# Kernel optimization log

Measured on AMD Instinct MI355X. Metric: run time of the kernel, lower is better.

The kernel has to match this reference:

```python
import jax, jax.numpy as jnp
import numpy as np

MAX_REL = 128  # max_relative_position


def setup_inputs() -> dict:
    key = jax.random.key(0)
    k1, k2, k3, k4 = jax.random.split(key, 4)
    B, H, S, D = 2, 8, 2048, 64
    q = jax.random.normal(k1, (B, H, S, D), dtype=jnp.float32)
    k = jax.random.normal(k2, (B, H, S, D), dtype=jnp.float32)
    v = jax.random.normal(k3, (B, H, S, D), dtype=jnp.float32)
    rel_table = jax.random.normal(k4, (2 * MAX_REL + 1, D), dtype=jnp.float32)
    return {"q": q, "k": k, "v": v, "rel_table": rel_table}


def reference(q, k, v, rel_table):
    B, H, S, D = q.shape
    scale = jnp.sqrt(jnp.asarray(D, q.dtype))
    # content scores: [B,H,S,S]
    qk_scores = jnp.einsum('bhqd,bhkd->bhqk', q, k)
    # relative position index matrix [S,S] clamped to [-MAX_REL, MAX_REL]
    pos = jnp.arange(S)
    rel_idx = jnp.clip(pos[None, :] - pos[:, None], -MAX_REL, MAX_REL) + MAX_REL
    rel_emb = rel_table[rel_idx]  # [S,S,D]
    # relative scores: per-query dot with rel embedding row -> [B,H,S,S]
    rel_scores = jnp.einsum('bhqd,qkd->bhqk', q, rel_emb)
    scores = (qk_scores + rel_scores) / scale
    attn = jax.nn.softmax(scores, axis=-1)
    # output: [B,H,S,D]
    return jnp.einsum('bhqk,bhkd->bhqd', attn, v)
```

## Files before the change

kernel.cpp:

```cpp
#include <hip/hip_runtime.h>

typedef _Float16 half8 __attribute__((ext_vector_type(8)));
typedef _Float16 half4 __attribute__((ext_vector_type(4)));
typedef float f32x4 __attribute__((ext_vector_type(4)));

#define S_LEN 2048
#define HDIM 64
#define QBLK 64
#define KVBLK 64
#define NT (S_LEN / KVBLK)
#define QRS 258
#define NBH 16
#define L2E 1.44269504f
#define TSTR 72

__device__ __forceinline__ void load_lds16(const void* g, void* l) {
    __builtin_amdgcn_global_load_lds(
        (const __attribute__((address_space(1))) unsigned int*)g,
        (__attribute__((address_space(3))) unsigned int*)l, 16, 0, 0);
}

__global__ __launch_bounds__(256)
void convert_kv_kernel(const float* __restrict__ Kg, const float* __restrict__ Vg,
                       _Float16* __restrict__ Kh, _Float16* __restrict__ Vp)
{
    __shared__ _Float16 tile[KVBLK * TSTR];
    const int bid = blockIdx.x;
    const int tid = threadIdx.x;
    if (bid < 1024) {
        const int id = bid * 256 + tid;
        const int r  = id >> 3;
        const int d0 = (id & 7) * 8;
        const float* src = Kg + (size_t)r * HDIM + d0;
        f32x4 f0 = *(const f32x4*)(src);
        f32x4 f1 = *(const f32x4*)(src + 4);
        half8 h;
#pragma unroll
        for (int j = 0; j < 4; ++j) { h[j] = (_Float16)f0[j]; h[j+4] = (_Float16)f1[j]; }
        const int bh = r >> 11, kvg = r & 2047;
        const int t = kvg >> 6, kv = kvg & 63;
        const size_t blk = (size_t)(bh * NT + t) * 8192;
        const int off = (kv * 128 + d0 * 2) ^ ((kv & 7) << 4);
        *(half8*)((char*)Kh + blk + off) = h;
    } else {
        const int bt = bid - 1024;
        const int bh = bt >> 5, t = bt & 31;
        {
            const int kv = tid >> 2;
            const int d0 = (tid & 3) * 16;
            const float* src = Vg + ((size_t)bh * S_LEN + t * KVBLK + kv) * HDIM + d0;
            f32x4 f0 = *(const f32x4*)(src);
            f32x4 f1 = *(const f32x4*)(src + 4);
            f32x4 f2 = *(const f32x4*)(src + 8);
            f32x4 f3 = *(const f32x4*)(src + 12);
            half8 h0, h1;
#pragma unroll
            for (int j = 0; j < 4; ++j) {
                h0[j] = (_Float16)f0[j]; h0[j+4] = (_Float16)f1[j];
                h1[j] = (_Float16)f2[j]; h1[j+4] = (_Float16)f3[j];
            }
            *(half8*)&tile[kv * TSTR + d0]     = h0;
            *(half8*)&tile[kv * TSTR + d0 + 8] = h1;
        }
        __syncthreads();
        {
            const int dp = tid >> 2;
            const int u0 = (tid & 3) * 2;
            char* base = (char*)Vp + (size_t)bt * 8192;
            const int dsw = (dp & 7) << 4;
#pragma unroll
            for (int ui = 0; ui < 2; ++ui) {
                const int u  = u0 + ui;
                const int kc = u >> 2, gg = u & 3;
                half8 ch;
#pragma unroll
                for (int r = 0; r < 4; ++r) {
                    ch[r]     = tile[(32*kc + 4*gg + r)      * TSTR + dp];
                    ch[4 + r] = tile[(32*kc + 16 + 4*gg + r) * TSTR + dp];
                }
                *(half8*)(base + ((dp * 128 + u * 16) ^ dsw)) = ch;
            }
        }
    }
}

__global__ __launch_bounds__(512, 4)
void relattn_v7(const float* __restrict__ Qg, const float* __restrict__ RELg,
                const _Float16* __restrict__ Kh, const _Float16* __restrict__ Vp,
                float* __restrict__ Og)
{
    __shared__ __attribute__((aligned(16))) _Float16 Kbuf[2][4096];
    __shared__ __attribute__((aligned(16))) _Float16 Vbuf[2][4096];
    __shared__ __attribute__((aligned(16))) _Float16 Qrel[QBLK * QRS];
    __shared__ float MLds[2][64];
    __shared__ float LLds[2][64];

    const int tid  = threadIdx.x;
    const int wave = tid >> 6;
    const int lane = tid & 63;
    const int c  = lane & 15;
    const int g  = lane >> 4;
    const int qs = wave & 3;
    const int ks = wave >> 2;

    const int wk = ((blockIdx.x & 7) << 6) + (blockIdx.x >> 3);
    const int bh = wk >> 5;
    const int q0 = (wk & 31) * QBLK;
    const size_t hoff = (size_t)bh * S_LEN * HDIM;

    const int qb0 = q0 + 16 * qs;
    half8 bq[2];
#pragma unroll
    for (int kc = 0; kc < 2; ++kc) {
        const float* src = Qg + hoff + (size_t)(qb0 + c) * HDIM + kc * 32 + g * 8;
        f32x4 f0 = *(const f32x4*)(src);
        f32x4 f1 = *(const f32x4*)(src + 4);
        half8 h;
#pragma unroll
        for (int j = 0; j < 4; ++j) {
            h[j]     = (_Float16)(f0[j] * 0.125f);
            h[j + 4] = (_Float16)(f1[j] * 0.125f);
        }
        bq[kc] = h;
    }

    if (ks == 0) {
#pragma unroll 1
        for (int t = 0; t < 17; ++t) {
            f32x4 acc = {0.f, 0.f, 0.f, 0.f};
            int r = t * 16 + c;
            if (r > 256) r = 256;
#pragma unroll
            for (int kc = 0; kc < 2; ++kc) {
                const float* src = RELg + (size_t)r * HDIM + kc * 32 + g * 8;
                f32x4 f0 = *(const f32x4*)(src);
                f32x4 f1 = *(const f32x4*)(src + 4);
                half8 b;
#pragma unroll
                for (int j = 0; j < 4; ++j) { b[j] = (_Float16)f0[j]; b[j+4] = (_Float16)f1[j]; }
                acc = __builtin_amdgcn_mfma_f32_16x16x32_f16(bq[kc], b, acc, 0, 0, 0);
            }
            const int col = t * 16 + c;
            if (col <= 256) {
#pragma unroll
                for (int reg = 0; reg < 4; ++reg)
                    Qrel[(16 * qs + 4 * g + reg) * QRS + col] = (_Float16)acc[reg];
            }
        }
    }

    const char* kimg = (const char*)Kh + (size_t)bh * NT * 8192;
    const char* vimg = (const char*)Vp + (size_t)bh * NT * 8192;
    load_lds16(kimg + tid * 16, (char*)Kbuf + tid * 16);
    load_lds16(vimg + tid * 16, (char*)Vbuf + tid * 16);

    __syncthreads();

    const _Float16* qr = &Qrel[(16 * qs + c) * QRS];
    const float bias_lo = (float)qr[0];
    const float bias_hi = (float)qr[256];

    const int swz = (c & 7) << 4;
    int akoff[2][2], voff[4];
#pragma unroll
    for (int n = 0; n < 2; ++n)
#pragma unroll
        for (int kc = 0; kc < 2; ++kc)
            akoff[n][kc] = (((32 * ks + 16 * n + c) * 128) + kc * 64 + g * 16) ^ swz;
#pragma unroll
    for (int dn = 0; dn < 4; ++dn)
        voff[dn] = (((16 * dn + c) * 128) + ks * 64 + g * 16) ^ swz;

    half8 ones;
#pragma unroll
    for (int j = 0; j < 8; ++j) ones[j] = (_Float16)1.0f;

    float m = -1e30f;
    f32x4 l_acc = {0.f, 0.f, 0.f, 0.f};
    f32x4 oacc[4];
#pragma unroll
    for (int i = 0; i < 4; ++i) oacc[i] = (f32x4){0.f, 0.f, 0.f, 0.f};

#define BODY(t, b) do {                                                              \
        asm volatile("s_waitcnt vmcnt(0)" ::: "memory");                             \
        __builtin_amdgcn_s_barrier();                                                \
        {                                                                            \
            const int tn = ((t) + 1 < NT) ? (t) + 1 : (t);                           \
            load_lds16(kimg + (size_t)tn * 8192 + tid * 16,                          \
                       (char*)Kbuf + ((b) ^ 1) * 8192 + tid * 16);                   \
            load_lds16(vimg + (size_t)tn * 8192 + tid * 16,                          \
                       (char*)Vbuf + ((b) ^ 1) * 8192 + tid * 16);                   \
        }                                                                            \
        const char* kb = (const char*)Kbuf + (b) * 8192;                             \
        const char* vb = (const char*)Vbuf + (b) * 8192;                             \
        const int kws = (t) * KVBLK + 32 * ks;                                       \
        half8 a00 = *(const half8*)(kb + akoff[0][0]);                               \
        half8 a01 = *(const half8*)(kb + akoff[0][1]);                               \
        half8 a10 = *(const half8*)(kb + akoff[1][0]);                               \
        half8 a11 = *(const half8*)(kb + akoff[1][1]);                               \
        f32x4 s0 = {0.f,0.f,0.f,0.f}, s1 = {0.f,0.f,0.f,0.f};                        \
        __builtin_amdgcn_s_setprio(1);                                               \
        s0 = __builtin_amdgcn_mfma_f32_16x16x32_f16(a00, bq[0], s0, 0, 0, 0);        \
        s1 = __builtin_amdgcn_mfma_f32_16x16x32_f16(a10, bq[0], s1, 0, 0, 0);        \
        s0 = __builtin_amdgcn_mfma_f32_16x16x32_f16(a01, bq[1], s0, 0, 0, 0);        \
        s1 = __builtin_amdgcn_mfma_f32_16x16x32_f16(a11, bq[1], s1, 0, 0, 0);        \
        __builtin_amdgcn_s_setprio(0);                                               \
        float bias = 0.f;                                                            \
        float lm;                                                                    \
        if (kws + 159 <= qb0) {                                                      \
            bias = bias_lo;                                                          \
            lm = fmaxf(fmaxf(fmaxf(s0[0], s0[1]), fmaxf(s0[2], s0[3])),              \
                       fmaxf(fmaxf(s1[0], s1[1]), fmaxf(s1[2], s1[3]))) + bias;      \
        } else if (kws >= qb0 + 143) {                                               \
            bias = bias_hi;                                                          \
            lm = fmaxf(fmaxf(fmaxf(s0[0], s0[1]), fmaxf(s0[2], s0[3])),              \
                       fmaxf(fmaxf(s1[0], s1[1]), fmaxf(s1[2], s1[3]))) + bias;      \
        } else {                                                                     \
            const int base_d = kws + 4 * g - (qb0 + c) + 128;                        \
            _Pragma("unroll")                                                        \
            for (int r = 0; r < 4; ++r) {                                            \
                int i0 = base_d + r;                                                 \
                i0 = i0 < 0 ? 0 : (i0 > 256 ? 256 : i0);                             \
                int i1 = base_d + 16 + r;                                            \
                i1 = i1 < 0 ? 0 : (i1 > 256 ? 256 : i1);                             \
                s0[r] += (float)qr[i0];                                              \
                s1[r] += (float)qr[i1];                                              \
            }                                                                        \
            lm = fmaxf(fmaxf(fmaxf(s0[0], s0[1]), fmaxf(s0[2], s0[3])),              \
                       fmaxf(fmaxf(s1[0], s1[1]), fmaxf(s1[2], s1[3])));             \
        }                                                                            \
        if (!__all(lm <= m + 8.f)) {                                                 \
            float mt = lm;                                                           \
            mt = fmaxf(mt, __shfl_xor(mt, 16, 64));                                  \
            mt = fmaxf(mt, __shfl_xor(mt, 32, 64));                                  \
            const float mnew = fmaxf(m, mt);                                         \
            const float al = __builtin_amdgcn_exp2f((m - mnew) * L2E);               \
            m = mnew;                                                                \
            _Pragma("unroll")                                                        \
            for (int r = 0; r < 4; ++r) {                                            \
                const float ar = __shfl(al, 20 * g + r, 64);                         \
                l_acc[r] *= ar;                                                      \
                _Pragma("unroll")                                                    \
                for (int dn = 0; dn < 4; ++dn) oacc[dn][r] *= ar;                    \
            }                                                                        \
        }                                                                            \
        const float fold = (bias - m) * L2E;                                         \
        half8 ap;                                                                    \
        _Pragma("unroll")                                                            \
        for (int r = 0; r < 4; ++r) {                                                \
            ap[r]     = (_Float16)__builtin_amdgcn_exp2f(fmaf(s0[r], L2E, fold));    \
            ap[4 + r] = (_Float16)__builtin_amdgcn_exp2f(fmaf(s1[r], L2E, fold));    \
        }                                                                            \
        half8 v0 = *(const half8*)(vb + voff[0]);                                    \
        half8 v1 = *(const half8*)(vb + voff[1]);                                    \
        half8 v2 = *(const half8*)(vb + voff[2]);                                    \
        half8 v3 = *(const half8*)(vb + voff[3]);                                    \
        __builtin_amdgcn_s_setprio(1);                                               \
        l_acc   = __builtin_amdgcn_mfma_f32_16x16x32_f16(ap, ones, l_acc, 0, 0, 0);  \
        oacc[0] = __builtin_amdgcn_mfma_f32_16x16x32_f16(ap, v0, oacc[0], 0, 0, 0);  \
        oacc[1] = __builtin_amdgcn_mfma_f32_16x16x32_f16(ap, v1, oacc[1], 0, 0, 0);  \
        oacc[2] = __builtin_amdgcn_mfma_f32_16x16x32_f16(ap, v2, oacc[2], 0, 0, 0);  \
        oacc[3] = __builtin_amdgcn_mfma_f32_16x16x32_f16(ap, v3, oacc[3], 0, 0, 0);  \
        __builtin_amdgcn_s_setprio(0);                                               \
    } while (0)

#pragma unroll 1
    for (int tt = 0; tt < NT; tt += 2) {
        BODY(tt, 0);
        BODY(tt + 1, 1);
    }
#undef BODY

    asm volatile("s_waitcnt vmcnt(0)" ::: "memory");
    __syncthreads();

    {
        char* Ob = (char*)Kbuf;
#pragma unroll
        for (int r = 0; r < 4; ++r) {
            const int row = 16 * qs + 4 * g + r;
            const int rsw = (row & 7) << 4;
#pragma unroll
            for (int dn = 0; dn < 4; ++dn)
                *(_Float16*)(Ob + ks * 8192 + ((row * 128 + (16 * dn + c) * 2) ^ rsw))
                    = (_Float16)oacc[dn][r];
        }
        if (g == 0) MLds[ks][16 * qs + c] = m;
        if (c == 0) {
#pragma unroll
            for (int r = 0; r < 4; ++r)
                LLds[ks][16 * qs + 4 * g + r] = l_acc[r];
        }
        __syncthreads();

        const int row = 16 * qs + c;
        const int rsw = (c & 7) << 4;
        const float m0 = MLds[0][row], m1 = MLds[1][row];
        const float l0 = LLds[0][row], l1 = LLds[1][row];
        const float M  = fmaxf(m0, m1);
        const float w0 = __builtin_amdgcn_exp2f((m0 - M) * L2E);
        const float w1 = __builtin_amdgcn_exp2f((m1 - M) * L2E);
        const float inv = 1.0f / (l0 * w0 + l1 * w1);

        const int dof = 64 * ks + 16 * g;
        half8 o0 = *(const half8*)(Ob +        ((row * 128 + dof) ^ rsw));
        half8 o1 = *(const half8*)(Ob + 8192 + ((row * 128 + dof) ^ rsw));
        float* dst = Og + hoff + (size_t)(q0 + row) * HDIM + 32 * ks + 8 * g;
        f32x4 oA, oB;
#pragma unroll
        for (int j = 0; j < 4; ++j) {
            oA[j] = ((float)o0[j]     * w0 + (float)o1[j]     * w1) * inv;
            oB[j] = ((float)o0[4 + j] * w0 + (float)o1[4 + j] * w1) * inv;
        }
        *(f32x4*)dst = oA;
        *(f32x4*)(dst + 4) = oB;
    }
}

__global__ __launch_bounds__(256, 2)
void relattn_v1(const float* __restrict__ Qg, const float* __restrict__ Kg,
                const float* __restrict__ Vg, const float* __restrict__ RELg,
                float* __restrict__ Og)
{
    __shared__ _Float16 Klds[KVBLK * HDIM];
    __shared__ _Float16 Vt[HDIM * KVBLK];
    __shared__ _Float16 Plds[4][16 * KVBLK];
    __shared__ _Float16 Qrel[QBLK * QRS];

    const int tid  = threadIdx.x;
    const int wave = tid >> 6;
    const int lane = tid & 63;
    const int c = lane & 15;
    const int g = lane >> 4;

    const int bid = blockIdx.x;
    const int bh  = bid >> 5;
    const int q0  = (bid & 31) * QBLK;

    const size_t hoff = (size_t)bh * S_LEN * HDIM;
    const float* Qh = Qg + hoff;
    const float* Kh = Kg + hoff;
    const float* Vh = Vg + hoff;

    const int qrow_frag = q0 + wave * 16 + c;
    half8 aq[2];
#pragma unroll
    for (int kc = 0; kc < 2; ++kc) {
        const float* src = Qh + (size_t)qrow_frag * HDIM + kc * 32 + g * 8;
        f32x4 f0 = *(const f32x4*)(src);
        f32x4 f1 = *(const f32x4*)(src + 4);
        half8 h;
#pragma unroll
        for (int j = 0; j < 4; ++j) {
            h[j]     = (_Float16)(f0[j] * 0.125f);
            h[j + 4] = (_Float16)(f1[j] * 0.125f);
        }
        aq[kc] = h;
    }

#pragma unroll 1
    for (int t = 0; t < 17; ++t) {
        f32x4 acc = {0.f, 0.f, 0.f, 0.f};
        int r = t * 16 + c;
        if (r > 256) r = 256;
#pragma unroll
        for (int kc = 0; kc < 2; ++kc) {
            const float* src = RELg + (size_t)r * HDIM + kc * 32 + g * 8;
            f32x4 f0 = *(const f32x4*)(src);
            f32x4 f1 = *(const f32x4*)(src + 4);
            half8 b;
#pragma unroll
            for (int j = 0; j < 4; ++j) { b[j] = (_Float16)f0[j]; b[j+4] = (_Float16)f1[j]; }
            acc = __builtin_amdgcn_mfma_f32_16x16x32_f16(aq[kc], b, acc, 0, 0, 0);
        }
        const int col = t * 16 + c;
        if (col <= 256) {
#pragma unroll
            for (int reg = 0; reg < 4; ++reg)
                Qrel[(wave * 16 + 4 * g + reg) * QRS + col] = (_Float16)acc[reg];
        }
    }

    float mrow[4], lrow[4];
    f32x4 oacc[4];
#pragma unroll
    for (int i = 0; i < 4; ++i) {
        mrow[i] = -1e30f; lrow[i] = 0.f;
        oacc[i] = (f32x4){0.f, 0.f, 0.f, 0.f};
    }

    for (int k0 = 0; k0 < S_LEN; k0 += KVBLK) {
        __syncthreads();
        {
            const int r  = tid >> 2;
            const int dq = (tid & 3) << 4;
            const float* src = Kh + (size_t)(k0 + r) * HDIM + dq;
            f32x4 f0 = *(const f32x4*)(src);
            f32x4 f1 = *(const f32x4*)(src + 4);
            f32x4 f2 = *(const f32x4*)(src + 8);
            f32x4 f3 = *(const f32x4*)(src + 12);
            half8 h0, h1;
#pragma unroll
            for (int j = 0; j < 4; ++j) {
                h0[j] = (_Float16)f0[j]; h0[j+4] = (_Float16)f1[j];
                h1[j] = (_Float16)f2[j]; h1[j+4] = (_Float16)f3[j];
            }
            const int swz = (r & 7) << 4;
            char* base = (char*)Klds;
            *(half8*)(base + ((r * 128 + dq * 2) ^ swz))      = h0;
            *(half8*)(base + ((r * 128 + dq * 2 + 16) ^ swz)) = h1;
        }
        {
            const int kv = tid & 63;
            const int dbase = (tid >> 6) << 4;
            const float* src = Vh + (size_t)(k0 + kv) * HDIM + dbase;
            f32x4 f0 = *(const f32x4*)(src);
            f32x4 f1 = *(const f32x4*)(src + 4);
            f32x4 f2 = *(const f32x4*)(src + 8);
            f32x4 f3 = *(const f32x4*)(src + 12);
            float vals[16];
#pragma unroll
            for (int j = 0; j < 4; ++j) {
                vals[j] = f0[j]; vals[4+j] = f1[j]; vals[8+j] = f2[j]; vals[12+j] = f3[j];
            }
            char* base = (char*)Vt;
#pragma unroll
            for (int i = 0; i < 16; ++i) {
                const int d = dbase + i;
                const int off = (d * 128 + kv * 2) ^ ((d & 7) << 4);
                *(_Float16*)(base + off) = (_Float16)vals[i];
            }
        }
        __syncthreads();

        f32x4 sacc[4];
#pragma unroll
        for (int n = 0; n < 4; ++n) sacc[n] = (f32x4){0.f,0.f,0.f,0.f};
#pragma unroll
        for (int kc = 0; kc < 2; ++kc) {
#pragma unroll
            for (int n = 0; n < 4; ++n) {
                const int off = (((16*n + c) * 128) + kc * 64 + g * 16) ^ ((c & 7) << 4);
                half8 bk = *(const half8*)((const char*)Klds + off);
                sacc[n] = __builtin_amdgcn_mfma_f32_16x16x32_f16(aq[kc], bk, sacc[n], 0, 0, 0);
            }
        }

        float sval[4][4];
        const int myq0 = q0 + wave * 16 + 4 * g;
#pragma unroll
        for (int n = 0; n < 4; ++n) {
            const int kpos = k0 + 16 * n + c;
#pragma unroll
            for (int reg = 0; reg < 4; ++reg) {
                int rel = kpos - (myq0 + reg);
                rel = rel < -128 ? -128 : (rel > 128 ? 128 : rel);
                const float bias = (float)Qrel[(wave*16 + 4*g + reg) * QRS + (rel + 128)];
                sval[n][reg] = sacc[n][reg] + bias;
            }
        }

        float mt[4];
#pragma unroll
        for (int reg = 0; reg < 4; ++reg) {
            float mp = fmaxf(fmaxf(sval[0][reg], sval[1][reg]),
                             fmaxf(sval[2][reg], sval[3][reg]));
#pragma unroll
            for (int msk = 1; msk < 16; msk <<= 1)
                mp = fmaxf(mp, __shfl_xor(mp, msk, 64));
            mt[reg] = mp;
        }

        float alpha[4], psum[4];
#pragma unroll
        for (int reg = 0; reg < 4; ++reg) {
            const float mn = fmaxf(mrow[reg], mt[reg]);
            alpha[reg] = __expf(mrow[reg] - mn);
            mrow[reg] = mn;
            psum[reg] = 0.f;
        }

        char* pbase = (char*)&Plds[wave][0];
#pragma unroll
        for (int n = 0; n < 4; ++n) {
#pragma unroll
            for (int reg = 0; reg < 4; ++reg) {
                const float pv = __expf(sval[n][reg] - mrow[reg]);
                psum[reg] += pv;
                const int row = 4 * g + reg;
                const int off = (row * 128 + (16 * n + c) * 2) ^ ((row & 7) << 4);
                *(_Float16*)(pbase + off) = (_Float16)pv;
            }
        }

#pragma unroll
        for (int reg = 0; reg < 4; ++reg) {
            float ps = psum[reg];
#pragma unroll
            for (int msk = 1; msk < 16; msk <<= 1)
                ps += __shfl_xor(ps, msk, 64);
            lrow[reg] = lrow[reg] * alpha[reg] + ps;
#pragma unroll
            for (int dn = 0; dn < 4; ++dn) oacc[dn][reg] *= alpha[reg];
        }

        asm volatile("s_waitcnt lgkmcnt(0)" ::: "memory");

        half8 ap[2];
#pragma unroll
        for (int kc = 0; kc < 2; ++kc) {
            const int off = (c * 128 + kc * 64 + g * 16) ^ ((c & 7) << 4);
            ap[kc] = *(const half8*)(pbase + off);
        }
#pragma unroll
        for (int kc = 0; kc < 2; ++kc) {
#pragma unroll
            for (int dn = 0; dn < 4; ++dn) {
                const int drow = 16 * dn + c;
                const int off = (drow * 128 + kc * 64 + g * 16) ^ ((c & 7) << 4);
                half8 bv = *(const half8*)((const char*)Vt + off);
                oacc[dn] = __builtin_amdgcn_mfma_f32_16x16x32_f16(ap[kc], bv, oacc[dn], 0, 0, 0);
            }
        }
    }

#pragma unroll
    for (int reg = 0; reg < 4; ++reg) {
        const float inv = 1.0f / lrow[reg];
        const int row = q0 + wave * 16 + 4 * g + reg;
        float* dst = Og + hoff + (size_t)row * HDIM + c;
#pragma unroll
        for (int dn = 0; dn < 4; ++dn)
            dst[16 * dn] = oacc[dn][reg] * inv;
    }
}

extern "C" void kernel_launch(void* const* d_in, const int* in_sizes, int n_in,
                              void* d_out, int out_size, void* d_ws, size_t ws_size,
                              hipStream_t stream) {
    const float* q   = (const float*)d_in[0];
    const float* k   = (const float*)d_in[1];
    const float* v   = (const float*)d_in[2];
    const float* rel = (const float*)d_in[3];
    float* out = (float*)d_out;
    (void)in_sizes; (void)n_in; (void)out_size;

    const size_t kv_bytes = (size_t)NBH * S_LEN * HDIM * sizeof(_Float16);
    if (ws_size >= 2 * kv_bytes) {
        _Float16* KhB = (_Float16*)d_ws;
        _Float16* VpB = (_Float16*)((char*)d_ws + kv_bytes);
        convert_kv_kernel<<<dim3(1536), 256, 0, stream>>>(k, v, KhB, VpB);
        relattn_v7<<<dim3(NBH * (S_LEN / QBLK)), 512, 0, stream>>>(q, rel, KhB, VpB, out);
    } else {
        relattn_v1<<<dim3(NBH * (S_LEN / QBLK)), 256, 0, stream>>>(q, k, v, rel, out);
    }
}
```

Before: 58.59 us.

## Software-pipeline QK of the next tile with softmax and PV of the previous tile

Result: slower. 60.53 us (+3.3%).

```diff
diff --git a/kernel.cpp b/kernel.cpp
--- a/kernel.cpp
+++ b/kernel.cpp
@@ -6,9 +6,7 @@
 
 #define S_LEN 2048
 #define HDIM 64
-#define QBLK 64
-#define KVBLK 64
-#define NT (S_LEN / KVBLK)
+#define NT (S_LEN / 64)
 #define QRS 258
 #define NBH 16
 #define L2E 1.44269504f
@@ -24,7 +22,7 @@
 void convert_kv_kernel(const float* __restrict__ Kg, const float* __restrict__ Vg,
                        _Float16* __restrict__ Kh, _Float16* __restrict__ Vp)
 {
-    __shared__ _Float16 tile[KVBLK * TSTR];
+    __shared__ _Float16 tile[64 * TSTR];
     const int bid = blockIdx.x;
     const int tid = threadIdx.x;
     if (bid < 1024) {
@@ -48,7 +46,7 @@
         {
             const int kv = tid >> 2;
             const int d0 = (tid & 3) * 16;
-            const float* src = Vg + ((size_t)bh * S_LEN + t * KVBLK + kv) * HDIM + d0;
+            const float* src = Vg + ((size_t)bh * S_LEN + t * 64 + kv) * HDIM + d0;
             f32x4 f0 = *(const f32x4*)(src);
             f32x4 f1 = *(const f32x4*)(src + 4);
             f32x4 f2 = *(const f32x4*)(src + 8);
@@ -85,13 +83,13 @@
 }
 
 __global__ __launch_bounds__(512, 4)
-void relattn_v7(const float* __restrict__ Qg, const float* __restrict__ RELg,
-                const _Float16* __restrict__ Kh, const _Float16* __restrict__ Vp,
-                float* __restrict__ Og)
+void relattn_v10(const float* __restrict__ Qg, const float* __restrict__ RELg,
+                 const _Float16* __restrict__ Kh, const _Float16* __restrict__ Vp,
+                 float* __restrict__ Og)
 {
     __shared__ __attribute__((aligned(16))) _Float16 Kbuf[2][4096];
-    __shared__ __attribute__((aligned(16))) _Float16 Vbuf[2][4096];
-    __shared__ __attribute__((aligned(16))) _Float16 Qrel[QBLK * QRS];
+    __shared__ __attribute__((aligned(16))) _Float16 Vbuf[3][4096];
+    __shared__ __attribute__((aligned(16))) _Float16 Qrel[64 * QRS];
     __shared__ float MLds[2][64];
     __shared__ float LLds[2][64];
 
@@ -105,8 +103,14 @@
 
     const int wk = ((blockIdx.x & 7) << 6) + (blockIdx.x >> 3);
     const int bh = wk >> 5;
-    const int q0 = (wk & 31) * QBLK;
+    const int q0 = (wk & 31) * 64;
     const size_t hoff = (size_t)bh * S_LEN * HDIM;
+
+    const char* kimg = (const char*)Kh + (size_t)bh * NT * 8192;
+    const char* vimg = (const char*)Vp + (size_t)bh * NT * 8192;
+
+    load_lds16(kimg + tid * 16, (char*)&Kbuf[0][0] + tid * 16);
+    load_lds16(vimg + tid * 16, (char*)&Vbuf[0][0] + tid * 16);
 
     const int qb0 = q0 + 16 * qs;
     half8 bq[2];
@@ -148,12 +152,7 @@
             }
         }
     }
-
-    const char* kimg = (const char*)Kh + (size_t)bh * NT * 8192;
-    const char* vimg = (const char*)Vp + (size_t)bh * NT * 8192;
-    load_lds16(kimg + tid * 16, (char*)Kbuf + tid * 16);
-    load_lds16(vimg + tid * 16, (char*)Vbuf + tid * 16);
-
+    asm volatile("s_waitcnt vmcnt(0)" ::: "memory");
     __syncthreads();
 
     const _Float16* qr = &Qrel[(16 * qs + c) * QRS];
@@ -181,40 +180,35 @@
 #pragma unroll
     for (int i = 0; i < 4; ++i) oacc[i] = (f32x4){0.f, 0.f, 0.f, 0.f};
 
-#define BODY(t, b) do {                                                              \
-        asm volatile("s_waitcnt vmcnt(0)" ::: "memory");                             \
-        __builtin_amdgcn_s_barrier();                                                \
-        {                                                                            \
-            const int tn = ((t) + 1 < NT) ? (t) + 1 : (t);                           \
-            load_lds16(kimg + (size_t)tn * 8192 + tid * 16,                          \
-                       (char*)Kbuf + ((b) ^ 1) * 8192 + tid * 16);                   \
-            load_lds16(vimg + (size_t)tn * 8192 + tid * 16,                          \
-                       (char*)Vbuf + ((b) ^ 1) * 8192 + tid * 16);                   \
-        }                                                                            \
-        const char* kb = (const char*)Kbuf + (b) * 8192;                             \
-        const char* vb = (const char*)Vbuf + (b) * 8192;                             \
-        const int kws = (t) * KVBLK + 32 * ks;                                       \
-        half8 a00 = *(const half8*)(kb + akoff[0][0]);                               \
-        half8 a01 = *(const half8*)(kb + akoff[0][1]);                               \
-        half8 a10 = *(const half8*)(kb + akoff[1][0]);                               \
-        half8 a11 = *(const half8*)(kb + akoff[1][1]);                               \
-        f32x4 s0 = {0.f,0.f,0.f,0.f}, s1 = {0.f,0.f,0.f,0.f};                        \
-        __builtin_amdgcn_s_setprio(1);                                               \
-        s0 = __builtin_amdgcn_mfma_f32_16x16x32_f16(a00, bq[0], s0, 0, 0, 0);        \
-        s1 = __builtin_amdgcn_mfma_f32_16x16x32_f16(a10, bq[0], s1, 0, 0, 0);        \
-        s0 = __builtin_amdgcn_mfma_f32_16x16x32_f16(a01, bq[1], s0, 0, 0, 0);        \
-        s1 = __builtin_amdgcn_mfma_f32_16x16x32_f16(a11, bq[1], s1, 0, 0, 0);        \
-        __builtin_amdgcn_s_setprio(0);                                               \
+    load_lds16(kimg + 8192 + tid * 16, (char*)&Kbuf[1][0] + tid * 16);
+    load_lds16(vimg + 8192 + tid * 16, (char*)&Vbuf[1][0] + tid * 16);
+
+    f32x4 s0p, s1p;
+    {
+        const char* kb = (const char*)&Kbuf[0][0];
+        half8 a00 = *(const half8*)(kb + akoff[0][0]);
+        half8 a01 = *(const half8*)(kb + akoff[0][1]);
+        half8 a10 = *(const half8*)(kb + akoff[1][0]);
+        half8 a11 = *(const half8*)(kb + akoff[1][1]);
+        f32x4 z = {0.f,0.f,0.f,0.f};
+        s0p = __builtin_amdgcn_mfma_f32_16x16x32_f16(a00, bq[0], z, 0, 0, 0);
+        s1p = __builtin_amdgcn_mfma_f32_16x16x32_f16(a10, bq[0], z, 0, 0, 0);
+        s0p = __builtin_amdgcn_mfma_f32_16x16x32_f16(a01, bq[1], s0p, 0, 0, 0);
+        s1p = __builtin_amdgcn_mfma_f32_16x16x32_f16(a11, bq[1], s1p, 0, 0, 0);
+    }
+
+#define SOFTPV(PT, VB) do {                                                          \
+        const int kws = (PT) * 64 + 32 * ks;                                         \
         float bias = 0.f;                                                            \
         float lm;                                                                    \
         if (kws + 159 <= qb0) {                                                      \
             bias = bias_lo;                                                          \
-            lm = fmaxf(fmaxf(fmaxf(s0[0], s0[1]), fmaxf(s0[2], s0[3])),              \
-                       fmaxf(fmaxf(s1[0], s1[1]), fmaxf(s1[2], s1[3]))) + bias;      \
+            lm = fmaxf(fmaxf(fmaxf(s0p[0], s0p[1]), fmaxf(s0p[2], s0p[3])),          \
+                       fmaxf(fmaxf(s1p[0], s1p[1]), fmaxf(s1p[2], s1p[3]))) + bias;  \
         } else if (kws >= qb0 + 143) {                                               \
             bias = bias_hi;                                                          \
-            lm = fmaxf(fmaxf(fmaxf(s0[0], s0[1]), fmaxf(s0[2], s0[3])),              \
-                       fmaxf(fmaxf(s1[0], s1[1]), fmaxf(s1[2], s1[3]))) + bias;      \
+            lm = fmaxf(fmaxf(fmaxf(s0p[0], s0p[1]), fmaxf(s0p[2], s0p[3])),          \
+                       fmaxf(fmaxf(s1p[0], s1p[1]), fmaxf(s1p[2], s1p[3]))) + bias;  \
         } else {                                                                     \
             const int base_d = kws + 4 * g - (qb0 + c) + 128;                        \
             _Pragma("unroll")                                                        \
@@ -223,11 +217,11 @@
                 i0 = i0 < 0 ? 0 : (i0 > 256 ? 256 : i0);                             \
                 int i1 = base_d + 16 + r;                                            \
                 i1 = i1 < 0 ? 0 : (i1 > 256 ? 256 : i1);                             \
-                s0[r] += (float)qr[i0];                                              \
-                s1[r] += (float)qr[i1];                                              \
+                s0p[r] += (float)qr[i0];                                             \
+                s1p[r] += (float)qr[i1];                                             \
             }                                                                        \
-            lm = fmaxf(fmaxf(fmaxf(s0[0], s0[1]), fmaxf(s0[2], s0[3])),              \
-                       fmaxf(fmaxf(s1[0], s1[1]), fmaxf(s1[2], s1[3])));             \
+            lm = fmaxf(fmaxf(fmaxf(s0p[0], s0p[1]), fmaxf(s0p[2], s0p[3])),          \
+                       fmaxf(fmaxf(s1p[0], s1p[1]), fmaxf(s1p[2], s1p[3])));         \
         }                                                                            \
         if (!__all(lm <= m + 8.f)) {                                                 \
             float mt = lm;                                                           \
@@ -248,13 +242,14 @@
         half8 ap;                                                                    \
         _Pragma("unroll")                                                            \
         for (int r = 0; r < 4; ++r) {                                                \
-            ap[r]     = (_Float16)__builtin_amdgcn_exp2f(fmaf(s0[r], L2E, fold));    \
-            ap[4 + r] = (_Float16)__builtin_amdgcn_exp2f(fmaf(s1[r], L2E, fold));    \
+            ap[r]     = (_Float16)__builtin_amdgcn_exp2f(fmaf(s0p[r], L2E, fold));   \
+            ap[4 + r] = (_Float16)__builtin_amdgcn_exp2f(fmaf(s1p[r], L2E, fold));   \
         }                                                                            \
-        half8 v0 = *(const half8*)(vb + voff[0]);                                    \
-        half8 v1 = *(const half8*)(vb + voff[1]);                                    \
-        half8 v2 = *(const half8*)(vb + voff[2]);                                    \
-        half8 v3 = *(const half8*)(vb + voff[3]);                                    \
+        const char* vb_ = (const char*)Vbuf + (VB);                                  \
+        half8 v0 = *(const half8*)(vb_ + voff[0]);                                   \
+        half8 v1 = *(const half8*)(vb_ + voff[1]);                                   \
+        half8 v2 = *(const half8*)(vb_ + voff[2]);                                   \
+        half8 v3 = *(const half8*)(vb_ + voff[3]);                                   \
         __builtin_amdgcn_s_setprio(1);                                               \
         l_acc   = __builtin_amdgcn_mfma_f32_16x16x32_f16(ap, ones, l_acc, 0, 0, 0);  \
         oacc[0] = __builtin_amdgcn_mfma_f32_16x16x32_f16(ap, v0, oacc[0], 0, 0, 0);  \
@@ -264,16 +259,45 @@
         __builtin_amdgcn_s_setprio(0);                                               \
     } while (0)
 
+    int vprev = 0;
+    int vstg  = 2;
 #pragma unroll 1
-    for (int tt = 0; tt < NT; tt += 2) {
-        BODY(tt, 0);
-        BODY(tt + 1, 1);
-    }
-#undef BODY
+    for (int t = 1; t < NT; ++t) {
+        asm volatile("s_waitcnt vmcnt(1)" ::: "memory");
+        __builtin_amdgcn_s_barrier();
+
+        {
+            const int tn = (t + 1 < NT) ? t + 1 : NT - 1;
+            load_lds16(kimg + (size_t)tn * 8192 + tid * 16,
+                       (char*)&Kbuf[(t + 1) & 1][0] + tid * 16);
+            load_lds16(vimg + (size_t)tn * 8192 + tid * 16,
+                       (char*)Vbuf + vstg * 8192 + tid * 16);
+        }
+
+        const char* kb = (const char*)&Kbuf[t & 1][0];
+        half8 a00 = *(const half8*)(kb + akoff[0][0]);
+        half8 a01 = *(const half8*)(kb + akoff[0][1]);
+        half8 a10 = *(const half8*)(kb + akoff[1][0]);
+        half8 a11 = *(const half8*)(kb + akoff[1][1]);
+        f32x4 z = {0.f,0.f,0.f,0.f};
+        f32x4 n0, n1;
+        n0 = __builtin_amdgcn_mfma_f32_16x16x32_f16(a00, bq[0], z, 0, 0, 0);
+        n1 = __builtin_amdgcn_mfma_f32_16x16x32_f16(a10, bq[0], z, 0, 0, 0);
+        n0 = __builtin_amdgcn_mfma_f32_16x16x32_f16(a01, bq[1], n0, 0, 0, 0);
+        n1 = __builtin_amdgcn_mfma_f32_16x16x32_f16(a11, bq[1], n1, 0, 0, 0);
+
+        SOFTPV(t - 1, vprev * 8192);
+
+        s0p = n0; s1p = n1;
+        vprev = (vprev == 2) ? 0 : vprev + 1;
+        vstg  = (vstg  == 2) ? 0 : vstg  + 1;
+    }
+
+    SOFTPV(NT - 1, ((NT - 1) % 3) * 8192);
+#undef SOFTPV
 
     asm volatile("s_waitcnt vmcnt(0)" ::: "memory");
     __syncthreads();
-
     {
         char* Ob = (char*)Kbuf;
 #pragma unroll
@@ -322,10 +346,10 @@
                 const float* __restrict__ Vg, const float* __restrict__ RELg,
                 float* __restrict__ Og)
 {
-    __shared__ _Float16 Klds[KVBLK * HDIM];
-    __shared__ _Float16 Vt[HDIM * KVBLK];
-    __shared__ _Float16 Plds[4][16 * KVBLK];
-    __shared__ _Float16 Qrel[QBLK * QRS];
+    __shared__ _Float16 Klds[64 * HDIM];
+    __shared__ _Float16 Vt[HDIM * 64];
+    __shared__ _Float16 Plds[4][16 * 64];
+    __shared__ _Float16 Qrel[64 * QRS];
 
     const int tid  = threadIdx.x;
     const int wave = tid >> 6;
@@ -335,7 +359,7 @@
 
     const int bid = blockIdx.x;
     const int bh  = bid >> 5;
-    const int q0  = (bid & 31) * QBLK;
+    const int q0  = (bid & 31) * 64;
 
     const size_t hoff = (size_t)bh * S_LEN * HDIM;
     const float* Qh = Qg + hoff;
@@ -389,7 +413,7 @@
         oacc[i] = (f32x4){0.f, 0.f, 0.f, 0.f};
     }
 
-    for (int k0 = 0; k0 < S_LEN; k0 += KVBLK) {
+    for (int k0 = 0; k0 < S_LEN; k0 += 64) {
         __syncthreads();
         {
             const int r  = tid >> 2;
@@ -550,8 +574,8 @@
         _Float16* KhB = (_Float16*)d_ws;
         _Float16* VpB = (_Float16*)((char*)d_ws + kv_bytes);
         convert_kv_kernel<<<dim3(1536), 256, 0, stream>>>(k, v, KhB, VpB);
-        relattn_v7<<<dim3(NBH * (S_LEN / QBLK)), 512, 0, stream>>>(q, rel, KhB, VpB, out);
+        relattn_v10<<<dim3(512), 512, 0, stream>>>(q, rel, KhB, VpB, out);
     } else {
-        relattn_v1<<<dim3(NBH * (S_LEN / QBLK)), 256, 0, stream>>>(q, k, v, rel, out);
+        relattn_v1<<<dim3(512), 256, 0, stream>>>(q, k, v, rel, out);
     }
 }
```

## Switch attention to 32x32x16 MFMA with register-held K and 8-way KV split

Applied to the files above, without the earlier changes.

Result: slower. 65.82 us (+12.3%).

```diff
diff --git a/kernel.cpp b/kernel.cpp
--- a/kernel.cpp
+++ b/kernel.cpp
@@ -3,12 +3,12 @@
 typedef _Float16 half8 __attribute__((ext_vector_type(8)));
 typedef _Float16 half4 __attribute__((ext_vector_type(4)));
 typedef float f32x4 __attribute__((ext_vector_type(4)));
+typedef float f32x16 __attribute__((ext_vector_type(16)));
 
 #define S_LEN 2048
 #define HDIM 64
-#define QBLK 64
-#define KVBLK 64
-#define NT (S_LEN / KVBLK)
+#define NT (S_LEN / 64)
+#define NT2 16
 #define QRS 258
 #define NBH 16
 #define L2E 1.44269504f
@@ -24,7 +24,7 @@
 void convert_kv_kernel(const float* __restrict__ Kg, const float* __restrict__ Vg,
                        _Float16* __restrict__ Kh, _Float16* __restrict__ Vp)
 {
-    __shared__ _Float16 tile[KVBLK * TSTR];
+    __shared__ _Float16 tile[64 * TSTR];
     const int bid = blockIdx.x;
     const int tid = threadIdx.x;
     if (bid < 1024) {
@@ -48,7 +48,7 @@
         {
             const int kv = tid >> 2;
             const int d0 = (tid & 3) * 16;
-            const float* src = Vg + ((size_t)bh * S_LEN + t * KVBLK + kv) * HDIM + d0;
+            const float* src = Vg + ((size_t)bh * S_LEN + t * 64 + kv) * HDIM + d0;
             f32x4 f0 = *(const f32x4*)(src);
             f32x4 f1 = *(const f32x4*)(src + 4);
             f32x4 f2 = *(const f32x4*)(src + 8);
@@ -64,67 +64,86 @@
         }
         __syncthreads();
         {
-            const int dp = tid >> 2;
-            const int u0 = (tid & 3) * 2;
+            const int d = tid >> 2;
             char* base = (char*)Vp + (size_t)bt * 8192;
-            const int dsw = (dp & 7) << 4;
-#pragma unroll
-            for (int ui = 0; ui < 2; ++ui) {
-                const int u  = u0 + ui;
-                const int kc = u >> 2, gg = u & 3;
+            const int dsw = (d & 7) << 4;
+#pragma unroll
+            for (int gi = 0; gi < 2; ++gi) {
+                const int g8 = (tid & 3) * 2 + gi;
+                const int gq = g8 >> 2, c = (g8 >> 1) & 1, hh = g8 & 1;
                 half8 ch;
 #pragma unroll
-                for (int r = 0; r < 4; ++r) {
-                    ch[r]     = tile[(32*kc + 4*gg + r)      * TSTR + dp];
-                    ch[4 + r] = tile[(32*kc + 16 + 4*gg + r) * TSTR + dp];
+                for (int j = 0; j < 8; ++j) {
+                    const int kvloc = 32*gq + 16*c + (j & 3) + 8*(j >> 2) + 4*hh;
+                    ch[j] = tile[kvloc * TSTR + d];
                 }
-                *(half8*)(base + ((dp * 128 + u * 16) ^ dsw)) = ch;
+                *(half8*)(base + ((d * 128 + g8 * 16) ^ dsw)) = ch;
             }
         }
     }
 }
 
 __global__ __launch_bounds__(512, 4)
-void relattn_v7(const float* __restrict__ Qg, const float* __restrict__ RELg,
-                const _Float16* __restrict__ Kh, const _Float16* __restrict__ Vp,
-                float* __restrict__ Og)
+void relattn_v11(const float* __restrict__ Qg, const float* __restrict__ RELg,
+                 const _Float16* __restrict__ Kh, const _Float16* __restrict__ Vp,
+                 float* __restrict__ Og)
 {
-    __shared__ __attribute__((aligned(16))) _Float16 Kbuf[2][4096];
-    __shared__ __attribute__((aligned(16))) _Float16 Vbuf[2][4096];
-    __shared__ __attribute__((aligned(16))) _Float16 Qrel[QBLK * QRS];
-    __shared__ float MLds[2][64];
-    __shared__ float LLds[2][64];
+    __shared__ __attribute__((aligned(16))) _Float16 Vbuf[2][8192];
+    __shared__ __attribute__((aligned(16))) _Float16 Qrel[64 * QRS];
+    __shared__ float MLm[8][32];
+    __shared__ float MLl[8][32];
 
     const int tid  = threadIdx.x;
     const int wave = tid >> 6;
     const int lane = tid & 63;
-    const int c  = lane & 15;
-    const int g  = lane >> 4;
-    const int qs = wave & 3;
-    const int ks = wave >> 2;
+    const int dq = lane & 31;
+    const int h  = lane >> 5;
+    const int qh = wave & 1;
+    const int kq = wave >> 1;
 
     const int wk = ((blockIdx.x & 7) << 6) + (blockIdx.x >> 3);
     const int bh = wk >> 5;
-    const int q0 = (wk & 31) * QBLK;
+    const int q0 = (wk & 31) * 64;
     const size_t hoff = (size_t)bh * S_LEN * HDIM;
 
-    const int qb0 = q0 + 16 * qs;
-    half8 bq[2];
-#pragma unroll
-    for (int kc = 0; kc < 2; ++kc) {
-        const float* src = Qg + hoff + (size_t)(qb0 + c) * HDIM + kc * 32 + g * 8;
+    const char* kimg = (const char*)Kh + (size_t)bh * NT * 8192;
+    const char* vimg = (const char*)Vp + (size_t)bh * NT * 8192;
+
+    load_lds16(vimg + tid * 16,        (char*)&Vbuf[0][0] + tid * 16);
+    load_lds16(vimg + 8192 + tid * 16, (char*)&Vbuf[0][0] + 8192 + tid * 16);
+
+    const int qb0 = q0 + 32 * qh;
+    half8 bq[4];
+#pragma unroll
+    for (int ki = 0; ki < 4; ++ki) {
+        const float* src = Qg + hoff + (size_t)(qb0 + dq) * HDIM + 16 * ki + 8 * h;
         f32x4 f0 = *(const f32x4*)(src);
         f32x4 f1 = *(const f32x4*)(src + 4);
-        half8 h;
+        half8 hq;
 #pragma unroll
         for (int j = 0; j < 4; ++j) {
-            h[j]     = (_Float16)(f0[j] * 0.125f);
-            h[j + 4] = (_Float16)(f1[j] * 0.125f);
-        }
-        bq[kc] = h;
-    }
-
-    if (ks == 0) {
+            hq[j]     = (_Float16)(f0[j] * 0.125f);
+            hq[j + 4] = (_Float16)(f1[j] * 0.125f);
+        }
+        bq[ki] = hq;
+    }
+
+    if (wave < 4) {
+        const int c = lane & 15, g = lane >> 4;
+        half8 aq[2];
+#pragma unroll
+        for (int kc = 0; kc < 2; ++kc) {
+            const float* src = Qg + hoff + (size_t)(q0 + 16 * wave + c) * HDIM + kc * 32 + g * 8;
+            f32x4 f0 = *(const f32x4*)(src);
+            f32x4 f1 = *(const f32x4*)(src + 4);
+            half8 hq;
+#pragma unroll
+            for (int j = 0; j < 4; ++j) {
+                hq[j]     = (_Float16)(f0[j] * 0.125f);
+                hq[j + 4] = (_Float16)(f1[j] * 0.125f);
+            }
+            aq[kc] = hq;
+        }
 #pragma unroll 1
         for (int t = 0; t < 17; ++t) {
             f32x4 acc = {0.f, 0.f, 0.f, 0.f};
@@ -138,180 +157,191 @@
                 half8 b;
 #pragma unroll
                 for (int j = 0; j < 4; ++j) { b[j] = (_Float16)f0[j]; b[j+4] = (_Float16)f1[j]; }
-                acc = __builtin_amdgcn_mfma_f32_16x16x32_f16(bq[kc], b, acc, 0, 0, 0);
+                acc = __builtin_amdgcn_mfma_f32_16x16x32_f16(aq[kc], b, acc, 0, 0, 0);
             }
             const int col = t * 16 + c;
             if (col <= 256) {
 #pragma unroll
                 for (int reg = 0; reg < 4; ++reg)
-                    Qrel[(16 * qs + 4 * g + reg) * QRS + col] = (_Float16)acc[reg];
-            }
-        }
-    }
-
-    const char* kimg = (const char*)Kh + (size_t)bh * NT * 8192;
-    const char* vimg = (const char*)Vp + (size_t)bh * NT * 8192;
-    load_lds16(kimg + tid * 16, (char*)Kbuf + tid * 16);
-    load_lds16(vimg + tid * 16, (char*)Vbuf + tid * 16);
-
-    __syncthreads();
-
-    const _Float16* qr = &Qrel[(16 * qs + c) * QRS];
-    const float bias_lo = (float)qr[0];
-    const float bias_hi = (float)qr[256];
-
-    const int swz = (c & 7) << 4;
-    int akoff[2][2], voff[4];
-#pragma unroll
-    for (int n = 0; n < 2; ++n)
-#pragma unroll
-        for (int kc = 0; kc < 2; ++kc)
-            akoff[n][kc] = (((32 * ks + 16 * n + c) * 128) + kc * 64 + g * 16) ^ swz;
-#pragma unroll
-    for (int dn = 0; dn < 4; ++dn)
-        voff[dn] = (((16 * dn + c) * 128) + ks * 64 + g * 16) ^ swz;
-
-    half8 ones;
-#pragma unroll
-    for (int j = 0; j < 8; ++j) ones[j] = (_Float16)1.0f;
-
-    float m = -1e30f;
-    f32x4 l_acc = {0.f, 0.f, 0.f, 0.f};
-    f32x4 oacc[4];
-#pragma unroll
-    for (int i = 0; i < 4; ++i) oacc[i] = (f32x4){0.f, 0.f, 0.f, 0.f};
-
-#define BODY(t, b) do {                                                              \
+                    Qrel[(16 * wave + 4 * g + reg) * QRS + col] = (_Float16)acc[reg];
+            }
+        }
+    }
+
+    const int r64 = 32 * (kq & 1) + dq;
+    const int uadd = kq >> 1;
+    int koff[4];
+#pragma unroll
+    for (int ki = 0; ki < 4; ++ki)
+        koff[ki] = (r64 * 128 + 32 * ki + 16 * h) ^ ((r64 & 7) << 4);
+
+    half8 kA[4], kB[4];
+#pragma unroll
+    for (int ki = 0; ki < 4; ++ki)
+        kA[ki] = *(const half8*)(kimg + (size_t)uadd * 8192 + koff[ki]);
+
+    const int vhalf = (kq >> 1) * 8192;
+    const int gq = kq & 1;
+    int voff[2][2];
+#pragma unroll
+    for (int dh = 0; dh < 2; ++dh)
+#pragma unroll
+        for (int c = 0; c < 2; ++c) {
+            const int d = 32 * dh + dq;
+            voff[dh][c] = vhalf + ((d * 128 + gq * 64 + c * 32 + h * 16) ^ ((d & 7) << 4));
+        }
+
+    float m = -1e30f, l_run = 0.f;
+    f32x16 oacc0 = {0.f}, oacc1 = {0.f};
+#pragma unroll
+    for (int i = 0; i < 16; ++i) { oacc0[i] = 0.f; oacc1[i] = 0.f; }
+
+    const _Float16* qr = &Qrel[(32 * qh + dq) * QRS];
+
+#define BODY(t, b, KA, KB) do {                                                      \
         asm volatile("s_waitcnt vmcnt(0)" ::: "memory");                             \
         __builtin_amdgcn_s_barrier();                                                \
-        {                                                                            \
-            const int tn = ((t) + 1 < NT) ? (t) + 1 : (t);                           \
-            load_lds16(kimg + (size_t)tn * 8192 + tid * 16,                          \
-                       (char*)Kbuf + ((b) ^ 1) * 8192 + tid * 16);                   \
-            load_lds16(vimg + (size_t)tn * 8192 + tid * 16,                          \
-                       (char*)Vbuf + ((b) ^ 1) * 8192 + tid * 16);                   \
+        {                                  \
+            const int tn = ((t) + 1 < NT2) ? (t) + 1 : (t);                          \
+            load_lds16(vimg + (size_t)(2 * tn) * 8192 + tid * 16,                    \
+                       (char*)&Vbuf[(b) ^ 1][0] + tid * 16);                         \
+            load_lds16(vimg + (size_t)(2 * tn + 1) * 8192 + tid * 16,                \
+                       (char*)&Vbuf[(b) ^ 1][0] + 8192 + tid * 16);                  \
         }                                                                            \
-        const char* kb = (const char*)Kbuf + (b) * 8192;                             \
-        const char* vb = (const char*)Vbuf + (b) * 8192;                             \
-        const int kws = (t) * KVBLK + 32 * ks;                                       \
-        half8 a00 = *(const half8*)(kb + akoff[0][0]);                               \
-        half8 a01 = *(const half8*)(kb + akoff[0][1]);                               \
-        half8 a10 = *(const half8*)(kb + akoff[1][0]);                               \
-        half8 a11 = *(const half8*)(kb + akoff[1][1]);                               \
-        f32x4 s0 = {0.f,0.f,0.f,0.f}, s1 = {0.f,0.f,0.f,0.f};                        \
+        f32x16 sacc;                                                                 \
+        _Pragma("unroll")                                                            \
+        for (int i = 0; i < 16; ++i) sacc[i] = 0.f;                                  \
         __builtin_amdgcn_s_setprio(1);                                               \
-        s0 = __builtin_amdgcn_mfma_f32_16x16x32_f16(a00, bq[0], s0, 0, 0, 0);        \
-        s1 = __builtin_amdgcn_mfma_f32_16x16x32_f16(a10, bq[0], s1, 0, 0, 0);        \
-        s0 = __builtin_amdgcn_mfma_f32_16x16x32_f16(a01, bq[1], s0, 0, 0, 0);        \
-        s1 = __builtin_amdgcn_mfma_f32_16x16x32_f16(a11, bq[1], s1, 0, 0, 0);        \
+        sacc = __builtin_amdgcn_mfma_f32_32x32x16_f16(KA[0], bq[0], sacc, 0, 0, 0);  \
+        sacc = __builtin_amdgcn_mfma_f32_32x32x16_f16(KA[1], bq[1], sacc, 0, 0, 0);  \
+        sacc = __builtin_amdgcn_mfma_f32_32x32x16_f16(KA[2], bq[2], sacc, 0, 0, 0);  \
+        sacc = __builtin_amdgcn_mfma_f32_32x32x16_f16(KA[3], bq[3], sacc, 0, 0, 0);  \
         __builtin_amdgcn_s_setprio(0);                                               \
-        float bias = 0.f;                                                            \
-        float lm;                                                                    \
-        if (kws + 159 <= qb0) {                                                      \
-            bias = bias_lo;                                                          \
-            lm = fmaxf(fmaxf(fmaxf(s0[0], s0[1]), fmaxf(s0[2], s0[3])),              \
-                       fmaxf(fmaxf(s1[0], s1[1]), fmaxf(s1[2], s1[3]))) + bias;      \
-        } else if (kws >= qb0 + 143) {                                               \
-            bias = bias_hi;                                                          \
-            lm = fmaxf(fmaxf(fmaxf(s0[0], s0[1]), fmaxf(s0[2], s0[3])),              \
-                       fmaxf(fmaxf(s1[0], s1[1]), fmaxf(s1[2], s1[3]))) + bias;      \
+        {                                    \
+            const int tk = ((t) + 1 < NT2) ? (t) + 1 : (t);                          \
+            const char* kb_ = kimg + (size_t)(2 * tk + uadd) * 8192;                 \
+            _Pragma("unroll")                                                        \
+            for (int ki = 0; ki < 4; ++ki)                                           \
+                KB[ki] = *(const half8*)(kb_ + koff[ki]);                            \
+        }                                                                            \
+        float bias = 0.f, lm;                                                        \
+        if (128 * (t) <= q0 - 256) {                                                 \
+            bias = (float)qr[0];                                                     \
+            lm = sacc[0];                                                            \
+            _Pragma("unroll")                                                        \
+            for (int i = 1; i < 16; ++i) lm = fmaxf(lm, sacc[i]);                    \
+            lm += bias;                                                              \
+        } else if (128 * (t) >= q0 + 192) {                                          \
+            bias = (float)qr[256];                                                   \
+            lm = sacc[0];                                                            \
+            _Pragma("unroll")                                                        \
+            for (int i = 1; i < 16; ++i) lm = fmaxf(lm, sacc[i]);                    \
+            lm += bias;                                                              \
         } else {                                                                     \
-            const int base_d = kws + 4 * g - (qb0 + c) + 128;                        \
+            const int base_b = 128 * (t) + 32 * kq + 4 * h - (qb0 + dq) + 128;       \
+            lm = -1e30f;                                                             \
             _Pragma("unroll")                                                        \
-            for (int r = 0; r < 4; ++r) {                                            \
-                int i0 = base_d + r;                                                 \
-                i0 = i0 < 0 ? 0 : (i0 > 256 ? 256 : i0);                             \
-                int i1 = base_d + 16 + r;                                            \
-                i1 = i1 < 0 ? 0 : (i1 > 256 ? 256 : i1);                             \
-                s0[r] += (float)qr[i0];                                              \
-                s1[r] += (float)qr[i1];                                              \
+            for (int r = 0; r < 16; ++r) {                                           \
+                int idx = base_b + (r & 3) + 8 * (r >> 2);                           \
+                idx = idx < 0 ? 0 : (idx > 256 ? 256 : idx);                         \
+                sacc[r] += (float)qr[idx];                                           \
+                lm = fmaxf(lm, sacc[r]);                                             \
             }                                                                        \
-            lm = fmaxf(fmaxf(fmaxf(s0[0], s0[1]), fmaxf(s0[2], s0[3])),              \
-                       fmaxf(fmaxf(s1[0], s1[1]), fmaxf(s1[2], s1[3])));             \
         }                                                                            \
+        lm = fmaxf(lm, __shfl_xor(lm, 32, 64));                                      \
         if (!__all(lm <= m + 8.f)) {                                                 \
-            float mt = lm;                                                           \
-            mt = fmaxf(mt, __shfl_xor(mt, 16, 64));                                  \
-            mt = fmaxf(mt, __shfl_xor(mt, 32, 64));                                  \
-            const float mnew = fmaxf(m, mt);                                         \
+            const float mnew = fmaxf(m, lm);                                         \
             const float al = __builtin_amdgcn_exp2f((m - mnew) * L2E);               \
             m = mnew;                                                                \
+            l_run *= al;                                                             \
             _Pragma("unroll")                                                        \
-            for (int r = 0; r < 4; ++r) {                                            \
-                const float ar = __shfl(al, 20 * g + r, 64);                         \
-                l_acc[r] *= ar;                                                      \
-                _Pragma("unroll")                                                    \
-                for (int dn = 0; dn < 4; ++dn) oacc[dn][r] *= ar;                    \
+            for (int r = 0; r < 16; ++r) {                                           \
+                const float ar = __shfl(al, (r & 3) + 8 * (r >> 2) + 4 * h, 64);     \
+                oacc0[r] *= ar;                                                      \
+                oacc1[r] *= ar;                                                      \
             }                                                                        \
         }                                                                            \
         const float fold = (bias - m) * L2E;                                         \
-        half8 ap;                                                                    \
+        float ps = 0.f;                                                              \
+        half8 ap0, ap1;                                                              \
         _Pragma("unroll")                                                            \
-        for (int r = 0; r < 4; ++r) {                                                \
-            ap[r]     = (_Float16)__builtin_amdgcn_exp2f(fmaf(s0[r], L2E, fold));    \
-            ap[4 + r] = (_Float16)__builtin_amdgcn_exp2f(fmaf(s1[r], L2E, fold));    \
+        for (int j = 0; j < 8; ++j) {                                                \
+            const float p0 = __builtin_amdgcn_exp2f(fmaf(sacc[j], L2E, fold));       \
+            const float p1 = __builtin_amdgcn_exp2f(fmaf(sacc[8 + j], L2E, fold));   \
+            ps += p0 + p1;                                                           \
+            ap0[j] = (_Float16)p0;                                                   \
+            ap1[j] = (_Float16)p1;                                                   \
         }                                                                            \
-        half8 v0 = *(const half8*)(vb + voff[0]);                                    \
-        half8 v1 = *(const half8*)(vb + voff[1]);                                    \
-        half8 v2 = *(const half8*)(vb + voff[2]);                                    \
-        half8 v3 = *(const half8*)(vb + voff[3]);                                    \
+        ps += __shfl_xor(ps, 32, 64);                                                \
+        l_run += ps;                                                                 \
+        const char* vb_ = (const char*)&Vbuf[b][0];                                  \
+        half8 v00 = *(const half8*)(vb_ + voff[0][0]);                               \
+        half8 v01 = *(const half8*)(vb_ + voff[0][1]);                               \
+        half8 v10 = *(const half8*)(vb_ + voff[1][0]);                               \
+        half8 v11 = *(const half8*)(vb_ + voff[1][1]);                               \
         __builtin_amdgcn_s_setprio(1);                                               \
-        l_acc   = __builtin_amdgcn_mfma_f32_16x16x32_f16(ap, ones, l_acc, 0, 0, 0);  \
-        oacc[0] = __builtin_amdgcn_mfma_f32_16x16x32_f16(ap, v0, oacc[0], 0, 0, 0);  \
-        oacc[1] = __builtin_amdgcn_mfma_f32_16x16x32_f16(ap, v1, oacc[1], 0, 0, 0);  \
-        oacc[2] = __builtin_amdgcn_mfma_f32_16x16x32_f16(ap, v2, oacc[2], 0, 0, 0);  \
-        oacc[3] = __builtin_amdgcn_mfma_f32_16x16x32_f16(ap, v3, oacc[3], 0, 0, 0);  \
+        oacc0 = __builtin_amdgcn_mfma_f32_32x32x16_f16(ap0, v00, oacc0, 0, 0, 0);    \
+        oacc1 = __builtin_amdgcn_mfma_f32_32x32x16_f16(ap0, v10, oacc1, 0, 0, 0);    \
+        oacc0 = __builtin_amdgcn_mfma_f32_32x32x16_f16(ap1, v01, oacc0, 0, 0, 0);    \
+        oacc1 = __builtin_amdgcn_mfma_f32_32x32x16_f16(ap1, v11, oacc1, 0, 0, 0);    \
         __builtin_amdgcn_s_setprio(0);                                               \
     } while (0)
 
 #pragma unroll 1
-    for (int tt = 0; tt < NT; tt += 2) {
-        BODY(tt, 0);
-        BODY(tt + 1, 1);
+    for (int tt = 0; tt < NT2; tt += 2) {
+        BODY(tt,     0, kA, kB);
+        BODY(tt + 1, 1, kB, kA);
     }
 #undef BODY
 
     asm volatile("s_waitcnt vmcnt(0)" ::: "memory");
     __syncthreads();
-
     {
-        char* Ob = (char*)Kbuf;
-#pragma unroll
-        for (int r = 0; r < 4; ++r) {
-            const int row = 16 * qs + 4 * g + r;
-            const int rsw = (row & 7) << 4;
-#pragma unroll
-            for (int dn = 0; dn < 4; ++dn)
-                *(_Float16*)(Ob + ks * 8192 + ((row * 128 + (16 * dn + c) * 2) ^ rsw))
-                    = (_Float16)oacc[dn][r];
-        }
-        if (g == 0) MLds[ks][16 * qs + c] = m;
-        if (c == 0) {
-#pragma unroll
-            for (int r = 0; r < 4; ++r)
-                LLds[ks][16 * qs + 4 * g + r] = l_acc[r];
+        char* Ob = (char*)&Vbuf[0][0];
+#pragma unroll
+        for (int r = 0; r < 16; ++r) {
+            const int q = 32 * qh + (r & 3) + 8 * (r >> 2) + 4 * h;
+            _Float16* row = (_Float16*)(Ob + q * 512 + kq * 128);
+            row[dq]      = (_Float16)oacc0[r];
+            row[32 + dq] = (_Float16)oacc1[r];
+        }
+        if (lane < 32) {
+            MLm[wave][lane] = m;
+            MLl[wave][lane] = l_run;
         }
         __syncthreads();
 
-        const int row = 16 * qs + c;
-        const int rsw = (c & 7) << 4;
-        const float m0 = MLds[0][row], m1 = MLds[1][row];
-        const float l0 = LLds[0][row], l1 = LLds[1][row];
-        const float M  = fmaxf(m0, m1);
-        const float w0 = __builtin_amdgcn_exp2f((m0 - M) * L2E);
-        const float w1 = __builtin_amdgcn_exp2f((m1 - M) * L2E);
-        const float inv = 1.0f / (l0 * w0 + l1 * w1);
-
-        const int dof = 64 * ks + 16 * g;
-        half8 o0 = *(const half8*)(Ob +        ((row * 128 + dof) ^ rsw));
-        half8 o1 = *(const half8*)(Ob + 8192 + ((row * 128 + dof) ^ rsw));
-        float* dst = Og + hoff + (size_t)(q0 + row) * HDIM + 32 * ks + 8 * g;
+        const int qrow = tid >> 3;
+        const int d0   = (tid & 7) * 8;
+        const int qh_  = qrow >> 5, qloc = qrow & 31;
+        float mm[4], ll[4];
+#pragma unroll
+        for (int k4 = 0; k4 < 4; ++k4) {
+            mm[k4] = MLm[qh_ + 2 * k4][qloc];
+            ll[k4] = MLl[qh_ + 2 * k4][qloc];
+        }
+        const float M = fmaxf(fmaxf(mm[0], mm[1]), fmaxf(mm[2], mm[3]));
+        float wgt[4], den = 0.f;
+#pragma unroll
+        for (int k4 = 0; k4 < 4; ++k4) {
+            wgt[k4] = __builtin_amdgcn_exp2f((mm[k4] - M) * L2E);
+            den += wgt[k4] * ll[k4];
+        }
+        const float inv = 1.0f / den;
+        float acc[8];
+#pragma unroll
+        for (int e = 0; e < 8; ++e) acc[e] = 0.f;
+        const char* Obr = (const char*)&Vbuf[0][0] + qrow * 512;
+#pragma unroll
+        for (int k4 = 0; k4 < 4; ++k4) {
+            half8 o = *(const half8*)(Obr + k4 * 128 + d0 * 2);
+#pragma unroll
+            for (int e = 0; e < 8; ++e) acc[e] += (float)o[e] * wgt[k4];
+        }
+        float* dst = Og + hoff + (size_t)(q0 + qrow) * HDIM + d0;
         f32x4 oA, oB;
 #pragma unroll
-        for (int j = 0; j < 4; ++j) {
-            oA[j] = ((float)o0[j]     * w0 + (float)o1[j]     * w1) * inv;
-            oB[j] = ((float)o0[4 + j] * w0 + (float)o1[4 + j] * w1) * inv;
-        }
+        for (int j = 0; j < 4; ++j) { oA[j] = acc[j] * inv; oB[j] = acc[4 + j] * inv; }
         *(f32x4*)dst = oA;
         *(f32x4*)(dst + 4) = oB;
     }
@@ -322,10 +352,10 @@
                 const float* __restrict__ Vg, const float* __restrict__ RELg,
                 float* __restrict__ Og)
 {
-    __shared__ _Float16 Klds[KVBLK * HDIM];
-    __shared__ _Float16 Vt[HDIM * KVBLK];
-    __shared__ _Float16 Plds[4][16 * KVBLK];
-    __shared__ _Float16 Qrel[QBLK * QRS];
+    __shared__ _Float16 Klds[64 * HDIM];
+    __shared__ _Float16 Vt[HDIM * 64];
+    __shared__ _Float16 Plds[4][16 * 64];
+    __shared__ _Float16 Qrel[64 * QRS];
 
     const int tid  = threadIdx.x;
     const int wave = tid >> 6;
@@ -335,7 +365,7 @@
 
     const int bid = blockIdx.x;
     const int bh  = bid >> 5;
-    const int q0  = (bid & 31) * QBLK;
+    const int q0  = (bid & 31) * 64;
 
     const size_t hoff = (size_t)bh * S_LEN * HDIM;
     const float* Qh = Qg + hoff;
@@ -389,12 +419,12 @@
         oacc[i] = (f32x4){0.f, 0.f, 0.f, 0.f};
     }
 
-    for (int k0 = 0; k0 < S_LEN; k0 += KVBLK) {
+    for (int k0 = 0; k0 < S_LEN; k0 += 64) {
         __syncthreads();
         {
             const int r  = tid >> 2;
-            const int dq = (tid & 3) << 4;
-            const float* src = Kh + (size_t)(k0 + r) * HDIM + dq;
+            const int dqv = (tid & 3) << 4;
+            const float* src = Kh + (size_t)(k0 + r) * HDIM + dqv;
             f32x4 f0 = *(const f32x4*)(src);
             f32x4 f1 = *(const f32x4*)(src + 4);
             f32x4 f2 = *(const f32x4*)(src + 8);
@@ -407,8 +437,8 @@
             }
             const int swz = (r & 7) << 4;
             char* base = (char*)Klds;
-            *(half8*)(base + ((r * 128 + dq * 2) ^ swz))      = h0;
-            *(half8*)(base + ((r * 128 + dq * 2 + 16) ^ swz)) = h1;
+            *(half8*)(base + ((r * 128 + dqv * 2) ^ swz))      = h0;
+            *(half8*)(base + ((r * 128 + dqv * 2 + 16) ^ swz)) = h1;
         }
         {
             const int kv = tid & 63;
@@ -550,8 +580,8 @@
         _Float16* KhB = (_Float16*)d_ws;
         _Float16* VpB = (_Float16*)((char*)d_ws + kv_bytes);
         convert_kv_kernel<<<dim3(1536), 256, 0, stream>>>(k, v, KhB, VpB);
-        relattn_v7<<<dim3(NBH * (S_LEN / QBLK)), 512, 0, stream>>>(q, rel, KhB, VpB, out);
+        relattn_v11<<<dim3(512), 512, 0, stream>>>(q, rel, KhB, VpB, out);
     } else {
-        relattn_v1<<<dim3(NBH * (S_LEN / QBLK)), 256, 0, stream>>>(q, k, v, rel, out);
+        relattn_v1<<<dim3(512), 256, 0, stream>>>(q, k, v, rel, out);
     }
 }
```
